# Performance work log

Measured on AMD Instinct MI355X. Metric: run time of the kernel, lower is better.

The kernel has to match this reference:

```python
import jax, jax.numpy as jnp
import numpy as np

B, S, D, H = 4, 2048, 512, 4
HD = D // H
EPS = 1e-5


def layer_norm(x, gamma, beta):
    mu = jnp.mean(x, axis=-1, keepdims=True)
    var = jnp.mean(jnp.square(x - mu), axis=-1, keepdims=True)
    return (x - mu) * jax.lax.rsqrt(var + EPS) * gamma + beta


def setup_inputs() -> dict:
    key = jax.random.key(0)
    ks = jax.random.split(key, 16)
    s_in = 1.0 / np.sqrt(D)
    s_ex = 1.0 / np.sqrt(2 * D)
    return {
        "input_states": jax.random.normal(ks[0], (B, S, D), jnp.float32),
        "positions": jax.random.normal(ks[1], (B, S, 3), jnp.float32),
        "W_expand": jax.random.uniform(ks[2], (D, 2 * D), jnp.float32, -s_in, s_in),
        "b_expand": jax.random.uniform(ks[3], (2 * D,), jnp.float32, -s_in, s_in),
        "W_squeeze": jax.random.uniform(ks[4], (2 * D, D), jnp.float32, -s_ex, s_ex),
        "b_squeeze": jax.random.uniform(ks[5], (D,), jnp.float32, -s_ex, s_ex),
        "gamma": jnp.ones((D,), jnp.float32),
        "beta": jnp.zeros((D,), jnp.float32),
        "Wq": jax.random.uniform(ks[6], (D, D), jnp.float32, -s_in, s_in),
        "bq": jax.random.uniform(ks[7], (D,), jnp.float32, -s_in, s_in),
        "Wk": jax.random.uniform(ks[8], (D, D), jnp.float32, -s_in, s_in),
        "bk": jax.random.uniform(ks[9], (D,), jnp.float32, -s_in, s_in),
        "Wv": jax.random.uniform(ks[10], (D, D), jnp.float32, -s_in, s_in),
        "bv": jax.random.uniform(ks[11], (D,), jnp.float32, -s_in, s_in),
        "alpha": jnp.float32(0.1),
    }


def reference(input_states, positions, W_expand, b_expand, W_squeeze, b_squeeze,
              gamma, beta, Wq, bq, Wk, bk, Wv, bv, alpha):
    # FFN (expand -> relu -> squeeze) + residual + LayerNorm
    h = jax.nn.relu(input_states @ W_expand + b_expand)
    squeezed = h @ W_squeeze + b_squeeze
    se = layer_norm(input_states + squeezed, gamma, beta)

    # q/k/v projections, split heads: [B,H,S,HD]
    q = (se @ Wq + bq).reshape(B, S, H, HD).transpose(0, 2, 1, 3)
    k = (se @ Wk + bk).reshape(B, S, H, HD).transpose(0, 2, 1, 3)
    v = (se @ Wv + bv).reshape(B, S, H, HD).transpose(0, 2, 1, 3)

    scores = jnp.einsum('bhid,bhjd->bhij', q, k) / np.sqrt(HD)

    # squared pairwise distance bias: ||pi||^2 + ||pj||^2 - 2 pi.pj, broadcast over heads
    sq = jnp.sum(positions * positions, axis=-1)  # [B,S]
    dist2 = sq[:, :, None] + sq[:, None, :] - 2.0 * jnp.einsum('bic,bjc->bij', positions, positions)
    dist2 = jnp.maximum(dist2, 0.0)
    scores = scores - alpha * dist2[:, None, :, :]

    w = jax.nn.softmax(scores, axis=-1)
    ctx = jnp.einsum('bhij,bhjd->bhid', w, v)
    ctx = ctx.transpose(0, 2, 1, 3).reshape(B, S, D)

    # same LayerNorm params reused (self.norm applied twice in original)
    return layer_norm(se + ctx, gamma, beta)
```

## Files before the change

### kernel.cpp

```cpp
#include <hip/hip_runtime.h>

typedef __bf16 bf16_t;
typedef __attribute__((ext_vector_type(8))) __bf16 bf16x8;
typedef __attribute__((ext_vector_type(4))) __bf16 bf16x4;
typedef __attribute__((ext_vector_type(4))) float f32x4;
typedef __attribute__((ext_vector_type(16))) float f32x16;

constexpr int Bc = 4, Sc = 2048, Dc = 512, Hc = 4, HDc = 128;
constexpr int Mrows = Bc * Sc;

__device__ inline void gl2lds(const void* g, void* l) {
  __builtin_amdgcn_global_load_lds(
      (__attribute__((address_space(1))) void*)g,
      (__attribute__((address_space(3))) void*)l, 16, 0, 0);
}

__global__ __launch_bounds__(256) void prep_k(
    const float* __restrict__ X, bf16_t* __restrict__ xb,
    const float* __restrict__ pos, const float* __restrict__ alphap,
    bf16_t* __restrict__ Qbg, bf16_t* __restrict__ Kbg,
    const float* __restrict__ We, bf16_t* __restrict__ wtE,
    const float* __restrict__ Ws, bf16_t* __restrict__ wtS,
    const float* __restrict__ Wq, const float* __restrict__ Wk,
    const float* __restrict__ Wv, bf16_t* __restrict__ wtQKV) {
  const int bid = blockIdx.x;
  if (bid < 2048) {
    const long i = ((long)bid * 256 + threadIdx.x) * 8;
    const float4 a = *(const float4*)(X + i);
    const float4 c = *(const float4*)(X + i + 4);
    bf16x8 o;
    o[0] = (bf16_t)a.x; o[1] = (bf16_t)a.y; o[2] = (bf16_t)a.z; o[3] = (bf16_t)a.w;
    o[4] = (bf16_t)c.x; o[5] = (bf16_t)c.y; o[6] = (bf16_t)c.z; o[7] = (bf16_t)c.w;
    *(bf16x8*)(xb + i) = o;
    return;
  }
  if (bid < 2080) {
    const float ap = alphap[0] * 11.313708498984761f;
    const int i = (bid - 2048) * 256 + threadIdx.x;
    const int b = i >> 11, s = i & 2047;
    const float x = pos[(long)i * 3], y = pos[(long)i * 3 + 1], z = pos[(long)i * 3 + 2];
    const float m2 = -ap * (x * x + y * y + z * z);
    bf16x8 qlo = {}, klo = {}, zer = {};
    qlo[0] = (bf16_t)(2.f * ap * x); qlo[1] = (bf16_t)(2.f * ap * y);
    qlo[2] = (bf16_t)(2.f * ap * z); qlo[3] = (bf16_t)1.0f;
    klo[0] = (bf16_t)x; klo[1] = (bf16_t)y; klo[2] = (bf16_t)z; klo[3] = (bf16_t)m2;
    *(bf16x8*)(Qbg + (long)i * 16) = qlo;
    *(bf16x8*)(Qbg + (long)i * 16 + 8) = zer;
    const int t = s >> 6, kh = (s >> 5) & 1, key = s & 31;
    const long kb = ((long)(b * 32 + t) * 2 + kh) * 512 + key * 8;
    *(bf16x8*)(Kbg + kb) = klo;
    *(bf16x8*)(Kbg + kb + 256) = zer;
    return;
  }
  __shared__ float tile[32][33];
  const float* src; bf16_t* dst; int K, N, local;
  if (bid < 2592)      { src = We; dst = wtE; K = 512;  N = 1024; local = bid - 2080; }
  else if (bid < 3104) { src = Ws; dst = wtS; K = 1024; N = 512;  local = bid - 2592; }
  else if (bid < 3360) { src = Wq; dst = wtQKV;          K = 512; N = 512; local = bid - 3104; }
  else if (bid < 3616) { src = Wk; dst = wtQKV + 262144; K = 512; N = 512; local = bid - 3360; }
  else                 { src = Wv; dst = wtQKV + 524288; K = 512; N = 512; local = bid - 3616; }
  const int nb = N / 32;
  const int n0 = (local % nb) * 32, k0 = (local / nb) * 32;
  const int tx = threadIdx.x & 31, ty = threadIdx.x >> 5;
#pragma unroll
  for (int i = 0; i < 4; i++)
    tile[ty + i * 8][tx] = src[(long)(k0 + ty + i * 8) * N + n0 + tx];
  __syncthreads();
#pragma unroll
  for (int i = 0; i < 4; i++)
    dst[(long)(n0 + ty + i * 8) * K + k0 + tx] = (bf16_t)tile[tx][ty + i * 8];
}

template <int OMODE, int TN, int NB>
__global__ __launch_bounds__(256, (TN == 128) ? 2 : 3) void gemm128_k(
    const bf16_t* __restrict__ A, const bf16_t* __restrict__ Bt,
    const float* __restrict__ bias0, const float* __restrict__ bias1,
    const float* __restrict__ bias2, void* __restrict__ out0,
    void* __restrict__ out1, void* __restrict__ out2, int N, int K) {
  __shared__ bf16_t As[2][128 * 64];
  __shared__ bf16_t Bs[2][TN * 64];
  constexpr int MT = (TN == 128) ? 4 : 2;
  constexpr int BI = (TN == 128) ? 4 : 2;
  constexpr int MW = (TN == 128) ? 64 : 32;
  const int t = threadIdx.x;
  const int p = blockIdx.x;
  const int slot = p >> 3;
  const int by = (p & 7) + 8 * (slot / NB);
  const int bx = slot % NB;
  const int n0 = bx * TN, m0 = by * 128;
  const int lane = t & 63, wave = t >> 6;
  const int quad = lane >> 4, ln = lane & 15;
  const int wm = (TN == 128) ? (wave >> 1) : wave;
  const int wn = (TN == 128) ? (wave & 1) : 0;
  const int l8 = lane >> 3, g = lane & 7;
  const bf16_t* aseg = A + (long)(m0 + wave * 32 + l8) * K + (g ^ l8) * 8;
  const bf16_t* bseg = Bt + (long)(n0 + wave * (BI * 8) + l8) * K + (g ^ l8) * 8;
  auto stage = [&](int buf, int k0) {
#pragma unroll
    for (int i = 0; i < 4; i++)
      gl2lds(aseg + (long)i * 8 * K + k0, &As[buf][(wave * 32 + i * 8) * 64]);
#pragma unroll
    for (int i = 0; i < BI; i++)
      gl2lds(bseg + (long)i * 8 * K + k0, &Bs[buf][(wave * BI * 8 + i * 8) * 64]);
  };
  f32x4 acc[MT][4] = {};
  stage(0, 0);
  const int niter = K / 64;
  for (int it = 0; it < niter; it++) {
    const int cur = it & 1;
    __syncthreads();
    if (it + 1 < niter) stage(1 - cur, (it + 1) * 64);
#pragma unroll
    for (int kc = 0; kc < 2; kc++) {
      bf16x8 af[MT], bfr[4];
#pragma unroll
      for (int mt = 0; mt < MT; mt++)
        af[mt] = *(const bf16x8*)&As[cur][(wm * MW + mt * 16 + ln) * 64 +
                                          (((kc * 4 + quad) ^ (ln & 7)) * 8)];
#pragma unroll
      for (int nt = 0; nt < 4; nt++)
        bfr[nt] = *(const bf16x8*)&Bs[cur][(wn * 64 + nt * 16 + ln) * 64 +
                                           (((kc * 4 + quad) ^ (ln & 7)) * 8)];
#pragma unroll
      for (int mt = 0; mt < MT; mt++)
#pragma unroll
        for (int nt = 0; nt < 4; nt++)
          acc[mt][nt] = __builtin_amdgcn_mfma_f32_16x16x32_bf16(af[mt], bfr[nt],
                                                                acc[mt][nt], 0, 0, 0);
    }
  }
#pragma unroll
  for (int nt = 0; nt < 4; nt++) {
    const int gcol = n0 + wn * 64 + nt * 16 + ln;
    if constexpr (OMODE == 0 || OMODE == 1) {
      const float bv = bias0[gcol];
      bf16_t* o = (bf16_t*)out0;
#pragma unroll
      for (int mt = 0; mt < MT; mt++)
#pragma unroll
        for (int r = 0; r < 4; r++) {
          const int grow = m0 + wm * MW + mt * 16 + quad * 4 + r;
          float vv = acc[mt][nt][r] + bv;
          if constexpr (OMODE == 0) vv = vv > 0.f ? vv : 0.f;
          o[(long)grow * N + gcol] = (bf16_t)vv;
        }
    } else {
      const int which = gcol >> 9, n = gcol & 511;
      const int hh = n >> 7, hd = n & 127;
      const float bv = (which == 0 ? bias0 : which == 1 ? bias1 : bias2)[n];
      bf16_t* o = (bf16_t*)(which == 0 ? out0 : which == 1 ? out1 : out2);
#pragma unroll
      for (int mt = 0; mt < MT; mt++)
#pragma unroll
        for (int r = 0; r < 4; r++) {
          const int grow = m0 + wm * MW + mt * 16 + quad * 4 + r;
          const int b = grow >> 11, s = grow & 2047;
          const float vv = acc[mt][nt][r] + bv;
          long idx;
          if (which == 0) {
            idx = ((long)((b * Hc + hh) * Sc + s)) * HDc + hd;
          } else if (which == 1) {
            const int tt = s >> 6, kh = (s >> 5) & 1, key = s & 31;
            const int c = hd >> 4, lk = key + 32 * ((hd >> 3) & 1), j = hd & 7;
            idx = ((((long)((b * Hc + hh) * 32 + tt) * 2 + kh) * 8 + c) * 64 + lk) * 8 + j;
          } else {
            const int tt = s >> 6, ht2 = hd >> 5, kc2 = (s & 63) >> 4;
            const int kl = s & 15;
            const int klp = (kl & 3) | ((kl & 4) << 1) | ((kl & 8) >> 1);
            const int lk = (hd & 31) + 32 * (klp >> 3), j = klp & 7;
            idx = ((((long)((b * Hc + hh) * 32 + tt) * 4 + ht2) * 4 + kc2) * 64 + lk) * 8 + j;
          }
          o[idx] = (bf16_t)vv;
        }
    }
  }
}

template <int AF32, int OF32>
__global__ __launch_bounds__(256) void ln_k(const void* __restrict__ xa,
                                            const bf16_t* __restrict__ xb,
                                            const float* __restrict__ gamma,
                                            const float* __restrict__ beta,
                                            void* __restrict__ out) {
  const int wave = threadIdx.x >> 6, lane = threadIdx.x & 63;
  const long row = (long)blockIdx.x * 4 + wave;
  const int col0 = lane * 8;
  float vv[8];
  float s = 0.f, s2 = 0.f;
  const bf16x8 vb = *(const bf16x8*)(xb + row * Dc + col0);
  if constexpr (AF32) {
    const float* a = (const float*)xa + row * Dc + col0;
    const float4 a0 = *(const float4*)a;
    const float4 a1 = *(const float4*)(a + 4);
    const float xs[8] = {a0.x, a0.y, a0.z, a0.w, a1.x, a1.y, a1.z, a1.w};
#pragma unroll
    for (int j = 0; j < 8; j++) vv[j] = xs[j] + (float)vb[j];
  } else {
    const bf16x8 va = *(const bf16x8*)((const bf16_t*)xa + row * Dc + col0);
#pragma unroll
    for (int j = 0; j < 8; j++) vv[j] = (float)va[j] + (float)vb[j];
  }
#pragma unroll
  for (int j = 0; j < 8; j++) { s += vv[j]; s2 += vv[j] * vv[j]; }
#pragma unroll
  for (int off = 1; off < 64; off <<= 1) {
    s += __shfl_xor(s, off, 64);
    s2 += __shfl_xor(s2, off, 64);
  }
  const float mu = s * (1.f / Dc);
  const float var = s2 * (1.f / Dc) - mu * mu;
  const float rstd = rsqrtf(var + 1e-5f);
  const float4 g0 = *(const float4*)(gamma + col0);
  const float4 g1 = *(const float4*)(gamma + col0 + 4);
  const float4 b0 = *(const float4*)(beta + col0);
  const float4 b1 = *(const float4*)(beta + col0 + 4);
  const float gs[8] = {g0.x, g0.y, g0.z, g0.w, g1.x, g1.y, g1.z, g1.w};
  const float bs[8] = {b0.x, b0.y, b0.z, b0.w, b1.x, b1.y, b1.z, b1.w};
  if constexpr (OF32) {
    float* o = (float*)out + row * Dc + col0;
    float4 o0, o1;
    o0.x = (vv[0] - mu) * rstd * gs[0] + bs[0];
    o0.y = (vv[1] - mu) * rstd * gs[1] + bs[1];
    o0.z = (vv[2] - mu) * rstd * gs[2] + bs[2];
    o0.w = (vv[3] - mu) * rstd * gs[3] + bs[3];
    o1.x = (vv[4] - mu) * rstd * gs[4] + bs[4];
    o1.y = (vv[5] - mu) * rstd * gs[5] + bs[5];
    o1.z = (vv[6] - mu) * rstd * gs[6] + bs[6];
    o1.w = (vv[7] - mu) * rstd * gs[7] + bs[7];
    *(float4*)o = o0; *(float4*)(o + 4) = o1;
  } else {
    bf16x8 ob;
#pragma unroll
    for (int j = 0; j < 8; j++) ob[j] = (bf16_t)((vv[j] - mu) * rstd * gs[j] + bs[j]);
    *(bf16x8*)((bf16_t*)out + row * Dc + col0) = ob;
  }
}

__global__ __launch_bounds__(512, 4) void attn_k(const bf16_t* __restrict__ q,
                                                 const bf16_t* __restrict__ Kg,
                                                 const bf16_t* __restrict__ Vg,
                                                 const bf16_t* __restrict__ Qbg,
                                                 const bf16_t* __restrict__ Kbg,
                                                 bf16_t* __restrict__ ctx) {
  __shared__ float Oc[8192];
  __shared__ float RsD[8][32];
  const int t = threadIdx.x;
  const int p = blockIdx.x;
  const int qt = (p >> 3) & 31;
  const int gg = (p & 7) + 8 * (p >> 8);
  const int h = gg & 3, b = gg >> 2;
  const int q0 = qt * 64;
  const int wave = t >> 6, lane = t & 63;
  const int l31 = lane & 31, hb = lane >> 5;
  const int rh = wave & 1, hh = (wave >> 1) & 1, kh = wave >> 2;
  const float scale_l2 = 1.4426950408889634f * 0.08838834764831845f;

  bf16x8 qf[8], qbf;
  const long qrow = (long)((b * Hc + h) * Sc + q0 + rh * 32 + l31);
#pragma unroll
  for (int c = 0; c < 8; c++)
    qf[c] = *(const bf16x8*)(q + qrow * HDc + c * 16 + hb * 8);
  qbf = *(const bf16x8*)(Qbg + (long)(b * Sc + q0 + rh * 32 + l31) * 16 + hb * 8);

  const bf16_t* kfb = Kg + (long)((b * Hc + h) * 32) * 8192 + (kh * 8) * 512 + lane * 8;
  const bf16_t* vfb = Vg + (long)((b * Hc + h) * 32) * 8192 + (hh * 2) * 2048 +
                      kh * 1024 + lane * 8;
  const bf16_t* kbb = Kbg + (long)(b * 32) * 1024 + kh * 512 + lane * 8;

  float rsl = 0.f;
  f32x16 accT[2] = {};

  for (int kt = 0; kt < 32; kt++) {
    const bf16_t* kt_k = kfb + (long)kt * 8192;
    f32x16 sacc = {};
    __builtin_amdgcn_s_setprio(1);
#pragma unroll
    for (int c = 0; c < 8; c++) {
      const bf16x8 kr = *(const bf16x8*)(kt_k + c * 512);
      sacc = __builtin_amdgcn_mfma_f32_32x32x16_bf16(kr, qf[c], sacc, 0, 0, 0);
    }
    {
      const bf16x8 kbr = *(const bf16x8*)(kbb + (long)kt * 1024);
      sacc = __builtin_amdgcn_mfma_f32_32x32x16_bf16(kbr, qbf, sacc, 0, 0, 0);
    }
    __builtin_amdgcn_s_setprio(0);
    float pe[16];
#pragma unroll
    for (int i = 0; i < 16; i++) {
      pe[i] = __builtin_amdgcn_exp2f(sacc[i] * scale_l2);
      rsl += pe[i];
    }
    bf16x8 pf0, pf1;
#pragma unroll
    for (int j = 0; j < 8; j++) { pf0[j] = (bf16_t)pe[j]; pf1[j] = (bf16_t)pe[8 + j]; }
    const bf16_t* vt = vfb + (long)kt * 8192;
    __builtin_amdgcn_s_setprio(1);
#pragma unroll
    for (int ht2 = 0; ht2 < 2; ht2++) {
      const bf16x8 v0 = *(const bf16x8*)(vt + ht2 * 2048);
      accT[ht2] = __builtin_amdgcn_mfma_f32_32x32x16_bf16(v0, pf0, accT[ht2], 0, 0, 0);
      const bf16x8 v1 = *(const bf16x8*)(vt + ht2 * 2048 + 512);
      accT[ht2] = __builtin_amdgcn_mfma_f32_32x32x16_bf16(v1, pf1, accT[ht2], 0, 0, 0);
    }
    __builtin_amdgcn_s_setprio(0);
  }
  __syncthreads();

  rsl += __shfl_xor(rsl, 32, 64);
  if (hb == 0) RsD[wave][l31] = rsl;
  if (kh == 1) {
    float* dst = &Oc[(rh + 2 * hh) * 2048];
#pragma unroll
    for (int ht2 = 0; ht2 < 2; ht2++)
#pragma unroll
      for (int r = 0; r < 16; r++)
        dst[(ht2 * 16 + r) * 64 + lane] = accT[ht2][r];
  }
  __syncthreads();
  if (kh == 0) {
    const float* src = &Oc[(rh + 2 * hh) * 2048];
#pragma unroll
    for (int ht2 = 0; ht2 < 2; ht2++)
#pragma unroll
      for (int r = 0; r < 16; r++)
        accT[ht2][r] += src[(ht2 * 16 + r) * 64 + lane];
    const float rinv = 1.f / (RsD[wave][l31] + RsD[wave + 4][l31]);
    const long orow = (long)(b * Sc + q0 + rh * 32 + l31);
#pragma unroll
    for (int ht2 = 0; ht2 < 2; ht2++)
#pragma unroll
      for (int g2 = 0; g2 < 4; g2++) {
        bf16x4 ov;
#pragma unroll
        for (int r0 = 0; r0 < 4; r0++)
          ov[r0] = (bf16_t)(accT[ht2][g2 * 4 + r0] * rinv);
        *(bf16x4*)(ctx + orow * Dc + h * HDc + (hh * 2 + ht2) * 32 + 8 * g2 + 4 * hb) = ov;
      }
  }
}

constexpr size_t SQB_OFF = 0;
constexpr size_t SEB_OFF = 8388608;
constexpr size_t Q_OFF = 16777216;
constexpr size_t K_OFF = 25165824;
constexpr size_t V_OFF = 33554432;
constexpr size_t XB_OFF = Q_OFF;
constexpr size_t H_OFF = K_OFF;
constexpr size_t QBG_OFF = 41943040;
constexpr size_t KBG_OFF = QBG_OFF + 262144;
constexpr size_t WTE_OFF = KBG_OFF + 262144;
constexpr size_t WTS_OFF = WTE_OFF + 1048576;
constexpr size_t WTQKV_OFF = WTS_OFF + 1048576;

extern "C" void kernel_launch(void* const* d_in, const int* in_sizes, int n_in,
                              void* d_out, int out_size, void* d_ws, size_t ws_size,
                              hipStream_t stream) {
  const float* X = (const float*)d_in[0];
  const float* pos = (const float*)d_in[1];
  const float* W_expand = (const float*)d_in[2];
  const float* b_expand = (const float*)d_in[3];
  const float* W_squeeze = (const float*)d_in[4];
  const float* b_squeeze = (const float*)d_in[5];
  const float* gamma = (const float*)d_in[6];
  const float* beta = (const float*)d_in[7];
  const float* Wq = (const float*)d_in[8];
  const float* bq = (const float*)d_in[9];
  const float* Wk = (const float*)d_in[10];
  const float* bk = (const float*)d_in[11];
  const float* Wv = (const float*)d_in[12];
  const float* bv = (const float*)d_in[13];
  const float* alphap = (const float*)d_in[14];

  char* ws = (char*)d_ws;
  bf16_t* sqb = (bf16_t*)(ws + SQB_OFF);
  bf16_t* ctxb = (bf16_t*)(ws + SQB_OFF);
  bf16_t* seb = (bf16_t*)(ws + SEB_OFF);
  bf16_t* qbg = (bf16_t*)(ws + QBG_OFF);
  bf16_t* kbg = (bf16_t*)(ws + KBG_OFF);
  bf16_t* qb = (bf16_t*)(ws + Q_OFF);
  bf16_t* kb = (bf16_t*)(ws + K_OFF);
  bf16_t* vb = (bf16_t*)(ws + V_OFF);
  bf16_t* xbb = (bf16_t*)(ws + XB_OFF);
  bf16_t* hb = (bf16_t*)(ws + H_OFF);
  bf16_t* wtE = (bf16_t*)(ws + WTE_OFF);
  bf16_t* wtS = (bf16_t*)(ws + WTS_OFF);
  bf16_t* wtQKV = (bf16_t*)(ws + WTQKV_OFF);

  prep_k<<<3872, 256, 0, stream>>>(X, xbb, pos, alphap, qbg, kbg,
                                   W_expand, wtE, W_squeeze, wtS, Wq, Wk, Wv, wtQKV);
  gemm128_k<0, 128, 8><<<512, 256, 0, stream>>>(
      xbb, wtE, b_expand, nullptr, nullptr, hb, nullptr, nullptr, 1024, 512);
  gemm128_k<1, 64, 8><<<512, 256, 0, stream>>>(
      hb, wtS, b_squeeze, nullptr, nullptr, sqb, nullptr, nullptr, 512, 1024);
  ln_k<1, 0><<<Mrows / 4, 256, 0, stream>>>(X, sqb, gamma, beta, seb);
  gemm128_k<2, 128, 12><<<768, 256, 0, stream>>>(
      seb, wtQKV, bq, bk, bv, qb, kb, vb, 1536, 512);
  attn_k<<<512, 512, 0, stream>>>(qb, kb, vb, qbg, kbg, ctxb);
  ln_k<0, 1><<<Mrows / 4, 256, 0, stream>>>(seb, ctxb, gamma, beta, (float*)d_out);

  (void)in_sizes; (void)n_in; (void)out_size; (void)ws_size;
}
```

Baseline: 260.9 us.

## Stage K/V tiles in LDS with double buffering and widen attention query tile

The attention kernel now loads each K/V/bias tile once per block into shared memory with global_load_lds, double-buffered so the next tile is fetched while the current one is computed. Each block handles 128 query rows instead of 64, and each wave covers the full head dimension, so the grid halves to 256 blocks. This cuts redundant per-wave global loads of K and V and raises reuse per fetched tile. In exchange it adds a barrier every iteration, raises register pressure with four accumulators (occupancy hint lowered to 2), and leaves fewer blocks than before to fill the GPU.

```diff
diff --git a/kernel.cpp b/kernel.cpp
--- a/kernel.cpp
+++ b/kernel.cpp
@@ -236,23 +236,23 @@
   }
 }
 
-__global__ __launch_bounds__(512, 4) void attn_k(const bf16_t* __restrict__ q,
+__global__ __launch_bounds__(512, 2) void attn_k(const bf16_t* __restrict__ q,
                                                  const bf16_t* __restrict__ Kg,
                                                  const bf16_t* __restrict__ Vg,
                                                  const bf16_t* __restrict__ Qbg,
                                                  const bf16_t* __restrict__ Kbg,
                                                  bf16_t* __restrict__ ctx) {
-  __shared__ float Oc[8192];
+  __shared__ bf16_t SMEM[2][17408];
   __shared__ float RsD[8][32];
   const int t = threadIdx.x;
   const int p = blockIdx.x;
-  const int qt = (p >> 3) & 31;
-  const int gg = (p & 7) + 8 * (p >> 8);
-  const int h = gg & 3, b = gg >> 2;
-  const int q0 = qt * 64;
+  const int qt = (p >> 3) & 15;
+  const int bh = (p & 7) + 8 * (p >> 7);
+  const int h = bh & 3, b = bh >> 2;
+  const int q0 = qt * 128;
   const int wave = t >> 6, lane = t & 63;
   const int l31 = lane & 31, hb = lane >> 5;
-  const int rh = wave & 1, hh = (wave >> 1) & 1, kh = wave >> 2;
+  const int rh = wave & 3, kh = wave >> 2;
   const float scale_l2 = 1.4426950408889634f * 0.08838834764831845f;
 
   bf16x8 qf[8], qbf;
@@ -262,25 +262,47 @@
     qf[c] = *(const bf16x8*)(q + qrow * HDc + c * 16 + hb * 8);
   qbf = *(const bf16x8*)(Qbg + (long)(b * Sc + q0 + rh * 32 + l31) * 16 + hb * 8);
 
-  const bf16_t* kfb = Kg + (long)((b * Hc + h) * 32) * 8192 + (kh * 8) * 512 + lane * 8;
-  const bf16_t* vfb = Vg + (long)((b * Hc + h) * 32) * 8192 + (hh * 2) * 2048 +
-                      kh * 1024 + lane * 8;
-  const bf16_t* kbb = Kbg + (long)(b * 32) * 1024 + kh * 512 + lane * 8;
+  const bf16_t* kbase = Kg + (long)((b * Hc + h) * 32) * 8192 + lane * 8;
+  const bf16_t* vbase = Vg + (long)((b * Hc + h) * 32) * 8192 + lane * 8;
+  const bf16_t* kbbase = Kbg + (long)(b * 32) * 1024 + lane * 8;
+  auto stage = [&](int buf, int kt) {
+    if (wave < 4) {
+#pragma unroll
+      for (int i = 0; i < 4; i++) {
+        const int seg = wave * 4 + i;
+        gl2lds(kbase + (long)kt * 8192 + seg * 512, &SMEM[buf][seg * 512]);
+      }
+      if (wave < 2)
+        gl2lds(kbbase + (long)kt * 1024 + wave * 512, &SMEM[buf][16384 + wave * 512]);
+    } else {
+#pragma unroll
+      for (int i = 0; i < 4; i++) {
+        const int seg = (wave - 4) * 4 + i;
+        gl2lds(vbase + (long)kt * 8192 + seg * 512, &SMEM[buf][8192 + seg * 512]);
+      }
+    }
+  };
+  stage(0, 0);
 
   float rsl = 0.f;
-  f32x16 accT[2] = {};
+  f32x16 accT[4] = {};
 
   for (int kt = 0; kt < 32; kt++) {
-    const bf16_t* kt_k = kfb + (long)kt * 8192;
+    const int cur = kt & 1;
+    __syncthreads();
+    if (kt < 31) stage(1 - cur, kt + 1);
+    const bf16_t* Kc = &SMEM[cur][(kh * 8) * 512 + lane * 8];
+    const bf16_t* Vc = &SMEM[cur][8192 + kh * 1024 + lane * 8];
+    const bf16_t* Kbc = &SMEM[cur][16384 + kh * 512 + lane * 8];
     f32x16 sacc = {};
     __builtin_amdgcn_s_setprio(1);
 #pragma unroll
     for (int c = 0; c < 8; c++) {
-      const bf16x8 kr = *(const bf16x8*)(kt_k + c * 512);
-      sacc = __builtin_amdgcn_mfma_f32_32x32x16_bf16(kr, qf[c], sacc, 0, 0, 0);
+      const bf16x8 kf = *(const bf16x8*)(Kc + c * 512);
+      sacc = __builtin_amdgcn_mfma_f32_32x32x16_bf16(kf, qf[c], sacc, 0, 0, 0);
     }
     {
-      const bf16x8 kbr = *(const bf16x8*)(kbb + (long)kt * 1024);
+      const bf16x8 kbr = *(const bf16x8*)(Kbc);
       sacc = __builtin_amdgcn_mfma_f32_32x32x16_bf16(kbr, qbf, sacc, 0, 0, 0);
     }
     __builtin_amdgcn_s_setprio(0);
@@ -293,14 +315,13 @@
     bf16x8 pf0, pf1;
 #pragma unroll
     for (int j = 0; j < 8; j++) { pf0[j] = (bf16_t)pe[j]; pf1[j] = (bf16_t)pe[8 + j]; }
-    const bf16_t* vt = vfb + (long)kt * 8192;
     __builtin_amdgcn_s_setprio(1);
 #pragma unroll
-    for (int ht2 = 0; ht2 < 2; ht2++) {
-      const bf16x8 v0 = *(const bf16x8*)(vt + ht2 * 2048);
-      accT[ht2] = __builtin_amdgcn_mfma_f32_32x32x16_bf16(v0, pf0, accT[ht2], 0, 0, 0);
-      const bf16x8 v1 = *(const bf16x8*)(vt + ht2 * 2048 + 512);
-      accT[ht2] = __builtin_amdgcn_mfma_f32_32x32x16_bf16(v1, pf1, accT[ht2], 0, 0, 0);
+    for (int ht = 0; ht < 4; ht++) {
+      const bf16x8 v0 = *(const bf16x8*)(Vc + ht * 2048);
+      accT[ht] = __builtin_amdgcn_mfma_f32_32x32x16_bf16(v0, pf0, accT[ht], 0, 0, 0);
+      const bf16x8 v1 = *(const bf16x8*)(Vc + ht * 2048 + 512);
+      accT[ht] = __builtin_amdgcn_mfma_f32_32x32x16_bf16(v1, pf1, accT[ht], 0, 0, 0);
     }
     __builtin_amdgcn_s_setprio(0);
   }
@@ -308,33 +329,34 @@
 
   rsl += __shfl_xor(rsl, 32, 64);
   if (hb == 0) RsD[wave][l31] = rsl;
+  float* Oc = (float*)&SMEM[0][0];
   if (kh == 1) {
-    float* dst = &Oc[(rh + 2 * hh) * 2048];
-#pragma unroll
-    for (int ht2 = 0; ht2 < 2; ht2++)
+    float* dst = Oc + rh * 4096;
+#pragma unroll
+    for (int ht = 0; ht < 4; ht++)
 #pragma unroll
       for (int r = 0; r < 16; r++)
-        dst[(ht2 * 16 + r) * 64 + lane] = accT[ht2][r];
+        dst[(ht * 16 + r) * 64 + lane] = accT[ht][r];
   }
   __syncthreads();
   if (kh == 0) {
-    const float* src = &Oc[(rh + 2 * hh) * 2048];
-#pragma unroll
-    for (int ht2 = 0; ht2 < 2; ht2++)
+    const float* src = Oc + rh * 4096;
+#pragma unroll
+    for (int ht = 0; ht < 4; ht++)
 #pragma unroll
       for (int r = 0; r < 16; r++)
-        accT[ht2][r] += src[(ht2 * 16 + r) * 64 + lane];
-    const float rinv = 1.f / (RsD[wave][l31] + RsD[wave + 4][l31]);
+        accT[ht][r] += src[(ht * 16 + r) * 64 + lane];
+    const float rinv = 1.f / (RsD[rh][l31] + RsD[rh + 4][l31]);
     const long orow = (long)(b * Sc + q0 + rh * 32 + l31);
 #pragma unroll
-    for (int ht2 = 0; ht2 < 2; ht2++)
+    for (int ht = 0; ht < 4; ht++)
 #pragma unroll
       for (int g2 = 0; g2 < 4; g2++) {
         bf16x4 ov;
 #pragma unroll
         for (int r0 = 0; r0 < 4; r0++)
-          ov[r0] = (bf16_t)(accT[ht2][g2 * 4 + r0] * rinv);
-        *(bf16x4*)(ctx + orow * Dc + h * HDc + (hh * 2 + ht2) * 32 + 8 * g2 + 4 * hb) = ov;
+          ov[r0] = (bf16_t)(accT[ht][g2 * 4 + r0] * rinv);
+        *(bf16x4*)(ctx + orow * Dc + h * HDc + ht * 32 + 8 * g2 + 4 * hb) = ov;
       }
   }
 }
@@ -395,7 +417,7 @@
   ln_k<1, 0><<<Mrows / 4, 256, 0, stream>>>(X, sqb, gamma, beta, seb);
   gemm128_k<2, 128, 12><<<768, 256, 0, stream>>>(
       seb, wtQKV, bq, bk, bv, qb, kb, vb, 1536, 512);
-  attn_k<<<512, 512, 0, stream>>>(qb, kb, vb, qbg, kbg, ctxb);
+  attn_k<<<256, 512, 0, stream>>>(qb, kb, vb, qbg, kbg, ctxb);
   ln_k<0, 1><<<Mrows / 4, 256, 0, stream>>>(seb, ctxb, gamma, beta, (float*)d_out);
 
   (void)in_sizes; (void)n_in; (void)out_size; (void)ws_size;
```

Result: faster. 214.0 us (-18.0%).
